# Kernel optimization log

Hardware: AMD Instinct MI355X
Metric: run time of the kernel (lower is better)

## Reference

```python
import jax, jax.numpy as jnp
import numpy as np

WIN = (2, 7, 7)
SHIFT = (1, 3, 3)
D, H, W = 8, 56, 56
C, NH = 128, 4
B = 8
N = WIN[0] * WIN[1] * WIN[2]  # 98


def _relative_position_index():
    d, h, w = np.meshgrid(np.arange(WIN[0]), np.arange(WIN[1]), np.arange(WIN[2]), indexing='ij')
    coords = np.stack([d.ravel(), h.ravel(), w.ravel()])  # (3, N)
    rel = coords[:, :, None] - coords[:, None, :]  # (3, N, N)
    rel = rel.transpose(1, 2, 0).astype(np.int64)
    rel[:, :, 0] += WIN[0] - 1
    rel[:, :, 1] += WIN[1] - 1
    rel[:, :, 2] += WIN[2] - 1
    rel[:, :, 0] *= (2 * WIN[1] - 1) * (2 * WIN[2] - 1)
    rel[:, :, 1] *= 2 * WIN[2] - 1
    return rel.sum(-1).astype(np.int32)  # (N, N)


def _shift_mask():
    img = np.zeros((1, D, H, W, 1), dtype=np.float32)
    cnt = 0
    for ds in (slice(0, -WIN[0]), slice(-WIN[0], -SHIFT[0]), slice(-SHIFT[0], None)):
        for hs in (slice(0, -WIN[1]), slice(-WIN[1], -SHIFT[1]), slice(-SHIFT[1], None)):
            for ws in (slice(0, -WIN[2]), slice(-WIN[2], -SHIFT[2]), slice(-SHIFT[2], None)):
                img[:, ds, hs, ws, :] = cnt
                cnt += 1
    m = img.reshape(1, D // WIN[0], WIN[0], H // WIN[1], WIN[1], W // WIN[2], WIN[2], 1)
    m = m.transpose(0, 1, 3, 5, 2, 4, 6, 7).reshape(-1, N)  # (nW, N)
    diff = m[:, None, :] - m[:, :, None]
    return np.where(diff != 0, np.float32(-100.0), np.float32(0.0))  # (nW, N, N)


def setup_inputs() -> dict:
    key = jax.random.key(0)
    ks = jax.random.split(key, 6)
    nW = (D // WIN[0]) * (H // WIN[1]) * (W // WIN[2])  # 256
    B_ = B * nW  # 2048
    table_size = (2 * WIN[0] - 1) * (2 * WIN[1] - 1) * (2 * WIN[2] - 1)  # 507
    return {
        'x': jax.random.normal(ks[0], (B_, N, C), dtype=jnp.float32),
        'qkv_w': jax.random.normal(ks[1], (3 * C, C), dtype=jnp.float32) * 0.02,
        'qkv_b': jax.random.normal(ks[2], (3 * C,), dtype=jnp.float32) * 0.02,
        'rpb_table': jax.random.normal(ks[3], (table_size, NH), dtype=jnp.float32) * 0.02,
        'proj_w': jax.random.normal(ks[4], (C, C), dtype=jnp.float32) * 0.02,
        'proj_b': jax.random.normal(ks[5], (C,), dtype=jnp.float32) * 0.02,
        'rel_index': jnp.asarray(_relative_position_index()),
        'mask': jnp.asarray(_shift_mask()),
    }


def reference(x, qkv_w, qkv_b, rpb_table, proj_w, proj_b, rel_index, mask):
    B_, n, c = x.shape
    hd = c // NH
    scale = hd ** -0.5
    # qkv projection -> (B_, n, 3, NH, hd)
    qkv = (x @ qkv_w.T + qkv_b).reshape(B_, n, 3, NH, hd)
    qkv = jnp.transpose(qkv, (2, 0, 3, 1, 4))  # (3, B_, NH, n, hd)
    q, k, v = qkv[0], qkv[1], qkv[2]
    attn = jnp.einsum('bhnd,bhmd->bhnm', q * scale, k)  # (B_, NH, n, n)
    # relative position bias gather
    bias = rpb_table[rel_index[:n, :n].reshape(-1)].reshape(n, n, NH)
    attn = attn + jnp.transpose(bias, (2, 0, 1))[None]
    # shift mask add
    nW = mask.shape[0]
    attn = attn.reshape(B_ // nW, nW, NH, n, n) + mask[None, :, None]
    attn = jax.nn.softmax(attn.reshape(B_, NH, n, n), axis=-1)
    out = jnp.einsum('bhnm,bhmd->bhnd', attn, v)
    out = jnp.transpose(out, (0, 2, 1, 3)).reshape(B_, n, c)
    return out @ proj_w.T + proj_b
```

## Files before the change

kernel.cpp:

```cpp
#include <hip/hip_runtime.h>
#include <math.h>
#include <stdint.h>


#define LOG2E   1.4426950408889634f
#define MASKNEG (-144.26950408889634f)

typedef __attribute__((ext_vector_type(8)))  short    bf16x8;
typedef __attribute__((ext_vector_type(4)))  float    f32x4;
typedef __attribute__((ext_vector_type(16))) float    f32x16;
typedef __attribute__((ext_vector_type(4)))  unsigned uint32x4;

__device__ __forceinline__ unsigned short cvt1(float f) {
    __bf16 h = (__bf16)f;
    return __builtin_bit_cast(unsigned short, h);
}
__device__ __forceinline__ unsigned cvt2(float lo, float hi) {
    return (unsigned)cvt1(lo) | ((unsigned)cvt1(hi) << 16);
}

__device__ __forceinline__ void pswap(unsigned &a, unsigned &b) {
    asm volatile("v_permlane32_swap_b32 %0, %1" : "+v"(a), "+v"(b));
}

__device__ __forceinline__ int tok_code(int t) {
    int pd = t / 49;
    int r  = t - pd * 49;
    int ph = r / 7;
    int pw = r - ph * 7;
    return (pd >= 1 ? 1 : 0) | (ph >= 4 ? 2 : 0) | (pw >= 4 ? 4 : 0);
}

__device__ __forceinline__ int swz2(int row, int col) {
    return row * 128 + ((((col >> 3) ^ (row & 7) ^ ((row >> 3) & 3)) & 15) << 3) + (col & 7);
}

template<bool BIG>
__global__ void prep_kernel(const float* __restrict__ qkv_w,
                            const float* __restrict__ proj_w,
                            const float* __restrict__ rpb_table,
                            const int*   __restrict__ rel_index,
                            unsigned short* __restrict__ wqkv,
                            unsigned short* __restrict__ wproj,
                            void* __restrict__ btab) {
    int tid = blockIdx.x * blockDim.x + threadIdx.x;
    int stride = gridDim.x * blockDim.x;
    for (int i = tid; i < 384 * 128; i += stride) wqkv[i]  = cvt1(qkv_w[i]);
    for (int i = tid; i < 128 * 128; i += stride) wproj[i] = cvt1(proj_w[i]);
    if constexpr (BIG) {
        float* bm = (float*)btab;
        for (int idx = tid; idx < 524288; idx += stride) {
            int e  = idx & 3;
            int il = (idx >> 2) & 31;
            int hi = (idx >> 7) & 1;
            int q  = (idx >> 8) & 3;
            int jt = (idx >> 10) & 3;
            int it = (idx >> 12) & 3;
            int h  = (idx >> 14) & 3;
            int cl = (idx >> 16);
            int i = it * 32 + il;
            int j = jt * 32 + q * 8 + hi * 4 + e;
            float v;
            if (j >= 98) v = -INFINITY;
            else if (i >= 98) v = 0.f;
            else {
                float bias = rpb_table[rel_index[i * 98 + j] * 4 + h];
                bool  msk  = (((unsigned)tok_code(i) ^ (unsigned)tok_code(j)) & (unsigned)cl) != 0;
                v = bias * LOG2E + (msk ? MASKNEG : 0.f);
            }
            bm[idx] = v;
        }
    } else {
        unsigned short* bm = (unsigned short*)btab;
        for (int idx = tid; idx < 65536; idx += stride) {
            int e  = idx & 3;
            int il = (idx >> 2) & 31;
            int hi = (idx >> 7) & 1;
            int q  = (idx >> 8) & 3;
            int jt = (idx >> 10) & 3;
            int it = (idx >> 12) & 3;
            int h  = (idx >> 14) & 3;
            int i = it * 32 + il;
            int j = jt * 32 + q * 8 + hi * 4 + e;
            float v;
            if (j >= 98) v = -INFINITY;
            else if (i >= 98) v = 0.f;
            else v = rpb_table[rel_index[i * 98 + j] * 4 + h] * LOG2E;
            bm[idx] = cvt1(v);
        }
    }
}

template<bool BIG>
__global__ __launch_bounds__(1024)
void swin_main(const float* __restrict__ x,
               const float* __restrict__ qkv_b,
               const float* __restrict__ proj_b,
               const unsigned short* __restrict__ wqkv,
               const unsigned short* __restrict__ wproj,
               const void* __restrict__ btab,
               float* __restrict__ out)
{
    extern __shared__ unsigned short lds[];
    unsigned short* q_lds  = lds;
    unsigned short* k_lds  = lds + 14336;
    unsigned short* vT_lds = lds + 28672;
    unsigned short* xo_lds = lds + 45056;

    const int b    = blockIdx.x;
    const int tid  = threadIdx.x;
    const int wv   = tid >> 6;
    const int lane = tid & 63;
    const int l4   = lane >> 4;
    const int lc   = lane & 15;

    {
        int idx2 = tid * 2;
        int row  = idx2 >> 4;
        int c    = 112 + (idx2 & 15);
        *(unsigned int*)(vT_lds + swz2(row, c)) = 0u;
    }

    {
        const float* xb = x + (size_t)b * 12544;
        for (int idx = tid; idx < 3584; idx += 1024) {
            int tok = idx >> 5;
            int c   = (idx & 31) << 2;
            float4 v;
            if (tok < 98) v = *(const float4*)(xb + tok * 128 + c);
            else { v.x = 0.f; v.y = 0.f; v.z = 0.f; v.w = 0.f; }
            uint2 hv; hv.x = cvt2(v.x, v.y); hv.y = cvt2(v.z, v.w);
            *(uint2*)(xo_lds + swz2(tok, c)) = hv;
        }
    }
    __syncthreads();

    {
        const int ct = wv;
        bf16x8 wf[4];
        f32x4  bias;
        const unsigned short* wrow = wqkv + (ct * 16 + lc) * 128;
#pragma unroll
        for (int kt = 0; kt < 4; ++kt) wf[kt] = *(const bf16x8*)(wrow + kt * 32 + l4 * 8);
#pragma unroll
        for (int r = 0; r < 4; ++r) bias[r] = qkv_b[ct * 16 + l4 * 4 + r];
        const bool  isq = (ct < 8);
        const float qs  = 0.17677669529663689f * LOG2E;
#pragma unroll
        for (int t = 0; t < 7; ++t) {
            bf16x8 xf[4];
#pragma unroll
            for (int kt = 0; kt < 4; ++kt)
                xf[kt] = *(bf16x8*)(xo_lds + swz2(t * 16 + lc, kt * 32 + l4 * 8));
            f32x4 acc = bias;
#pragma unroll
            for (int kt = 0; kt < 4; ++kt)
                acc = __builtin_amdgcn_mfma_f32_16x16x32_bf16(wf[kt], xf[kt], acc, 0, 0, 0);
            int tok = t * 16 + lc;
            if (isq) {
                uint2 hv; hv.x = cvt2(acc[0] * qs, acc[1] * qs); hv.y = cvt2(acc[2] * qs, acc[3] * qs);
                *(uint2*)(q_lds + swz2(tok, ct * 16 + l4 * 4)) = hv;
            } else {
                uint2 hv; hv.x = cvt2(acc[0], acc[1]); hv.y = cvt2(acc[2], acc[3]);
                *(uint2*)(k_lds + swz2(tok, (ct - 8) * 16 + l4 * 4)) = hv;
            }
        }
        const int vd = (wv >> 1) * 16;
        bf16x8 wf2[4];
        const unsigned short* wrow2 = wqkv + (256 + vd + lc) * 128;
#pragma unroll
        for (int kt = 0; kt < 4; ++kt) wf2[kt] = *(const bf16x8*)(wrow2 + kt * 32 + l4 * 8);
        f32x4 bias2;
#pragma unroll
        for (int r = 0; r < 4; ++r) bias2[r] = qkv_b[256 + vd + l4 * 4 + r];
        const int t0 = (wv & 1) ? 4 : 0, t1 = (wv & 1) ? 7 : 4;
        for (int t = t0; t < t1; ++t) {
            bf16x8 xf[4];
#pragma unroll
            for (int kt = 0; kt < 4; ++kt)
                xf[kt] = *(bf16x8*)(xo_lds + swz2(t * 16 + lc, kt * 32 + l4 * 8));
            f32x4 acc = bias2;
#pragma unroll
            for (int kt = 0; kt < 4; ++kt)
                acc = __builtin_amdgcn_mfma_f32_16x16x32_bf16(wf2[kt], xf[kt], acc, 0, 0, 0);
            int tok = t * 16 + lc;
            const int rb = vd + l4 * 4;
            vT_lds[swz2(rb + 0, tok)] = cvt1(acc[0]);
            vT_lds[swz2(rb + 1, tok)] = cvt1(acc[1]);
            vT_lds[swz2(rb + 2, tok)] = cvt1(acc[2]);
            vT_lds[swz2(rb + 3, tok)] = cvt1(acc[3]);
        }
    }
    __syncthreads();

    const int wi  = b & 255;
    const unsigned int cls =
        ((wi >> 6) == 3 ? 1u : 0u) | (((wi >> 3) & 7) == 7 ? 2u : 0u) | ((wi & 7) == 7 ? 4u : 0u);
    {
        const int il  = lane & 31;
        const int hi2 = lane >> 5;
        const int h     = wv >> 2;
        const int itile = wv & 3;
        const int i_tok = itile * 32 + il;

        f32x16 S[4];
        if constexpr (BIG) {
            const float* tb = (const float*)btab
                + (((size_t)(cls * 4 + h) * 4 + itile) * 4) * 1024 + hi2 * 128 + il * 4;
#pragma unroll
            for (int jt = 0; jt < 4; ++jt)
#pragma unroll
                for (int q = 0; q < 4; ++q) {
                    f32x4 v = *(const f32x4*)(tb + (jt * 8 + q * 2) * 128);
                    S[jt][q * 4 + 0] = v[0]; S[jt][q * 4 + 1] = v[1];
                    S[jt][q * 4 + 2] = v[2]; S[jt][q * 4 + 3] = v[3];
                }
        } else {
            const unsigned short* tb = (const unsigned short*)btab
                + ((h * 4 + itile) * 4) * 1024 + hi2 * 128 + il * 4;
            const unsigned int ci = (unsigned)tok_code(i_tok);
#pragma unroll
            for (int jt = 0; jt < 4; ++jt)
#pragma unroll
                for (int q = 0; q < 4; ++q) {
                    ushort4 bb = *(const ushort4*)(tb + (jt * 8 + q * 2) * 128);
#pragma unroll
                    for (int e = 0; e < 4; ++e) {
                        unsigned short us = (e == 0) ? bb.x : (e == 1) ? bb.y : (e == 2) ? bb.z : bb.w;
                        int j = jt * 32 + q * 8 + hi2 * 4 + e;
                        float mv = (((unsigned)tok_code(j) ^ ci) & cls) ? MASKNEG : 0.f;
                        S[jt][q * 4 + e] = __builtin_bit_cast(float, (unsigned)us << 16) + mv;
                    }
                }
        }

        bf16x8 qfa = *(bf16x8*)(q_lds + swz2(i_tok, h * 32 + hi2 * 8));
        bf16x8 qfb = *(bf16x8*)(q_lds + swz2(i_tok, h * 32 + 16 + hi2 * 8));
#pragma unroll
        for (int jt = 0; jt < 4; ++jt) {
            bf16x8 ka = *(bf16x8*)(k_lds + swz2(jt * 32 + il, h * 32 + hi2 * 8));
            bf16x8 kb = *(bf16x8*)(k_lds + swz2(jt * 32 + il, h * 32 + 16 + hi2 * 8));
            S[jt] = __builtin_amdgcn_mfma_f32_32x32x16_bf16(ka, qfa, S[jt], 0, 0, 0);
            S[jt] = __builtin_amdgcn_mfma_f32_32x32x16_bf16(kb, qfb, S[jt], 0, 0, 0);
        }

        float m = S[0][0];
#pragma unroll
        for (int jt = 0; jt < 4; ++jt)
#pragma unroll
            for (int r = 0; r < 16; ++r)
                if (!(jt == 0 && r == 0)) m = fmaxf(m, S[jt][r]);
        m = fmaxf(m, __shfl_xor(m, 32));

        float l = 0.f;
        unsigned dw[4][8];
#pragma unroll
        for (int jt = 0; jt < 4; ++jt)
#pragma unroll
            for (int d = 0; d < 8; ++d) {
                float p0 = exp2f(S[jt][2 * d]     - m);
                float p1 = exp2f(S[jt][2 * d + 1] - m);
                l += p0 + p1;
                dw[jt][d] = cvt2(p0, p1);
            }
        l += __shfl_xor(l, 32);

#pragma unroll
        for (int jt = 0; jt < 4; ++jt) {
            pswap(dw[jt][0], dw[jt][2]);
            pswap(dw[jt][1], dw[jt][3]);
            pswap(dw[jt][4], dw[jt][6]);
            pswap(dw[jt][5], dw[jt][7]);
        }

        f32x16 O = {0.f,0.f,0.f,0.f,0.f,0.f,0.f,0.f,0.f,0.f,0.f,0.f,0.f,0.f,0.f,0.f};
#pragma unroll
        for (int jt = 0; jt < 4; ++jt)
#pragma unroll
            for (int p = 0; p < 2; ++p) {
                bf16x8 vf = *(bf16x8*)(vT_lds + swz2(h * 32 + il, jt * 32 + p * 16 + hi2 * 8));
                uint32x4 pu = { dw[jt][p * 4 + 0], dw[jt][p * 4 + 1],
                                dw[jt][p * 4 + 2], dw[jt][p * 4 + 3] };
                O = __builtin_amdgcn_mfma_f32_32x32x16_bf16(
                        vf, __builtin_bit_cast(bf16x8, pu), O, 0, 0, 0);
            }

        const float inv = 1.0f / l;
#pragma unroll
        for (int rr = 0; rr < 8; ++rr) {
            int r = rr * 2;
            int d = (r & 3) + 8 * (r >> 2) + 4 * hi2;
            *(unsigned*)(xo_lds + swz2(i_tok, h * 32 + d)) = cvt2(O[r] * inv, O[r + 1] * inv);
        }
    }
    __syncthreads();

    {
        const int ct = wv >> 1;
        bf16x8 pw[4];
#pragma unroll
        for (int kt = 0; kt < 4; ++kt)
            pw[kt] = *(const bf16x8*)(wproj + (ct * 16 + lc) * 128 + kt * 32 + l4 * 8);
        f32x4 pbias;
#pragma unroll
        for (int r = 0; r < 4; ++r) pbias[r] = proj_b[ct * 16 + l4 * 4 + r];

        float* ob = out + (size_t)b * 12544;
        const int t0 = (wv & 1) ? 4 : 0, t1 = (wv & 1) ? 7 : 4;
        for (int t = t0; t < t1; ++t) {
            f32x4 acc = pbias;
#pragma unroll
            for (int kt = 0; kt < 4; ++kt) {
                bf16x8 of = *(bf16x8*)(xo_lds + swz2(t * 16 + lc, kt * 32 + l4 * 8));
                acc = __builtin_amdgcn_mfma_f32_16x16x32_bf16(pw[kt], of, acc, 0, 0, 0);
            }
            int tok = t * 16 + lc;
            if (tok < 98) {
                float4 st; st.x = acc[0]; st.y = acc[1]; st.z = acc[2]; st.w = acc[3];
                *(float4*)(ob + tok * 128 + ct * 16 + l4 * 4) = st;
            }
        }
    }
}

extern "C" void kernel_launch(void* const* d_in, const int* in_sizes, int n_in,
                              void* d_out, int out_size, void* d_ws, size_t ws_size,
                              hipStream_t stream) {
    const float* x       = (const float*)d_in[0];
    const float* qkv_w   = (const float*)d_in[1];
    const float* qkv_b   = (const float*)d_in[2];
    const float* rpb_tab = (const float*)d_in[3];
    const float* proj_w  = (const float*)d_in[4];
    const float* proj_b  = (const float*)d_in[5];
    const int*   rel_idx = (const int*)d_in[6];

    unsigned short* wqkv  = (unsigned short*)d_ws;
    unsigned short* wproj = (unsigned short*)((char*)d_ws + 98304);
    void*           btab  = (void*)((char*)d_ws + 131072);
    float*          out   = (float*)d_out;

    const bool big = ws_size >= (size_t)(131072 + 524288 * 4);
    const int LDS_BYTES = 122880;

    if (big) {
        hipLaunchKernelGGL((prep_kernel<true>), dim3(512), dim3(256), 0, stream,
                           qkv_w, proj_w, rpb_tab, rel_idx, wqkv, wproj, btab);
        (void)hipFuncSetAttribute((const void*)(swin_main<true>),
                                  hipFuncAttributeMaxDynamicSharedMemorySize, LDS_BYTES);
        hipLaunchKernelGGL((swin_main<true>), dim3(2048), dim3(1024), LDS_BYTES, stream,
                           x, qkv_b, proj_b, wqkv, wproj, btab, out);
    } else {
        hipLaunchKernelGGL((prep_kernel<false>), dim3(512), dim3(256), 0, stream,
                           qkv_w, proj_w, rpb_tab, rel_idx, wqkv, wproj, btab);
        (void)hipFuncSetAttribute((const void*)(swin_main<false>),
                                  hipFuncAttributeMaxDynamicSharedMemorySize, LDS_BYTES);
        hipLaunchKernelGGL((swin_main<false>), dim3(2048), dim3(1024), LDS_BYTES, stream,
                           x, qkv_b, proj_b, wqkv, wproj, btab, out);
    }
}
```

Baseline: 151.1 us.

## Process two windows per 1024-thread block with per-window 512-thread halves

Restructures the main kernel so each 1024-thread block handles two windows, each on 8 waves. Each wave computes Q, K and V for one 16-column slice in a single pass and keeps V in registers before writing it transposed. It also reuses LDS regions, skips the padded key tiles in softmax and PV, and drops the small-workspace fallback path. The goal is to halve the block count and amortize weight loads and synchronisation across more work. The cost is more LDS per block, about 158 KB, plus higher register pressure, and the code now assumes the large workspace is always available.

```diff
diff --git a/kernel.cpp b/kernel.cpp
--- a/kernel.cpp
+++ b/kernel.cpp
@@ -18,11 +18,9 @@
 __device__ __forceinline__ unsigned cvt2(float lo, float hi) {
     return (unsigned)cvt1(lo) | ((unsigned)cvt1(hi) << 16);
 }
-
 __device__ __forceinline__ void pswap(unsigned &a, unsigned &b) {
     asm volatile("v_permlane32_swap_b32 %0, %1" : "+v"(a), "+v"(b));
 }
-
 __device__ __forceinline__ int tok_code(int t) {
     int pd = t / 49;
     int r  = t - pd * 49;
@@ -30,183 +28,157 @@
     int pw = r - ph * 7;
     return (pd >= 1 ? 1 : 0) | (ph >= 4 ? 2 : 0) | (pw >= 4 ? 4 : 0);
 }
-
 __device__ __forceinline__ int swz2(int row, int col) {
     return row * 128 + ((((col >> 3) ^ (row & 7) ^ ((row >> 3) & 3)) & 15) << 3) + (col & 7);
 }
 
-template<bool BIG>
-__global__ void prep_kernel(const float* __restrict__ qkv_w,
-                            const float* __restrict__ proj_w,
-                            const float* __restrict__ rpb_table,
-                            const int*   __restrict__ rel_index,
-                            unsigned short* __restrict__ wqkv,
-                            unsigned short* __restrict__ wproj,
-                            void* __restrict__ btab) {
+__global__ void prep(const float* __restrict__ qkv_w,
+                     const float* __restrict__ proj_w,
+                     const float* __restrict__ rpb_table,
+                     const int*   __restrict__ rel_index,
+                     unsigned short* __restrict__ wqkv,
+                     unsigned short* __restrict__ wproj,
+                     float* __restrict__ bm) {
     int tid = blockIdx.x * blockDim.x + threadIdx.x;
     int stride = gridDim.x * blockDim.x;
     for (int i = tid; i < 384 * 128; i += stride) wqkv[i]  = cvt1(qkv_w[i]);
     for (int i = tid; i < 128 * 128; i += stride) wproj[i] = cvt1(proj_w[i]);
-    if constexpr (BIG) {
-        float* bm = (float*)btab;
-        for (int idx = tid; idx < 524288; idx += stride) {
-            int e  = idx & 3;
-            int il = (idx >> 2) & 31;
-            int hi = (idx >> 7) & 1;
-            int q  = (idx >> 8) & 3;
-            int jt = (idx >> 10) & 3;
-            int it = (idx >> 12) & 3;
-            int h  = (idx >> 14) & 3;
-            int cl = (idx >> 16);
-            int i = it * 32 + il;
-            int j = jt * 32 + q * 8 + hi * 4 + e;
-            float v;
-            if (j >= 98) v = -INFINITY;
-            else if (i >= 98) v = 0.f;
-            else {
-                float bias = rpb_table[rel_index[i * 98 + j] * 4 + h];
-                bool  msk  = (((unsigned)tok_code(i) ^ (unsigned)tok_code(j)) & (unsigned)cl) != 0;
-                v = bias * LOG2E + (msk ? MASKNEG : 0.f);
-            }
-            bm[idx] = v;
-        }
-    } else {
-        unsigned short* bm = (unsigned short*)btab;
-        for (int idx = tid; idx < 65536; idx += stride) {
-            int e  = idx & 3;
-            int il = (idx >> 2) & 31;
-            int hi = (idx >> 7) & 1;
-            int q  = (idx >> 8) & 3;
-            int jt = (idx >> 10) & 3;
-            int it = (idx >> 12) & 3;
-            int h  = (idx >> 14) & 3;
-            int i = it * 32 + il;
-            int j = jt * 32 + q * 8 + hi * 4 + e;
-            float v;
-            if (j >= 98) v = -INFINITY;
-            else if (i >= 98) v = 0.f;
-            else v = rpb_table[rel_index[i * 98 + j] * 4 + h] * LOG2E;
-            bm[idx] = cvt1(v);
-        }
-    }
-}
-
-template<bool BIG>
-__global__ __launch_bounds__(1024)
-void swin_main(const float* __restrict__ x,
-               const float* __restrict__ qkv_b,
-               const float* __restrict__ proj_b,
-               const unsigned short* __restrict__ wqkv,
-               const unsigned short* __restrict__ wproj,
-               const void* __restrict__ btab,
-               float* __restrict__ out)
+    for (int idx = tid; idx < 524288; idx += stride) {
+        int e  = idx & 3;
+        int il = (idx >> 2) & 31;
+        int hi = (idx >> 7) & 1;
+        int q  = (idx >> 8) & 3;
+        int jt = (idx >> 10) & 3;
+        int it = (idx >> 12) & 3;
+        int h  = (idx >> 14) & 3;
+        int cl = (idx >> 16);
+        int i = it * 32 + il;
+        int j = jt * 32 + q * 8 + hi * 4 + e;
+        float v;
+        if (j >= 98) v = -INFINITY;
+        else if (i >= 98) v = 0.f;
+        else {
+            float bias = rpb_table[rel_index[i * 98 + j] * 4 + h];
+            bool  msk  = (((unsigned)tok_code(i) ^ (unsigned)tok_code(j)) & (unsigned)cl) != 0;
+            v = bias * LOG2E + (msk ? MASKNEG : 0.f);
+        }
+        bm[idx] = v;
+    }
+}
+
+__global__ __launch_bounds__(1024, 4)
+void swin_fused2(const float* __restrict__ x,
+                 const float* __restrict__ qkv_b,
+                 const float* __restrict__ proj_b,
+                 const unsigned short* __restrict__ wqkv,
+                 const unsigned short* __restrict__ wproj,
+                 const float* __restrict__ bm,
+                 float* __restrict__ out)
 {
     extern __shared__ unsigned short lds[];
-    unsigned short* q_lds  = lds;
-    unsigned short* k_lds  = lds + 14336;
-    unsigned short* vT_lds = lds + 28672;
-    unsigned short* xo_lds = lds + 45056;
-
-    const int b    = blockIdx.x;
     const int tid  = threadIdx.x;
-    const int wv   = tid >> 6;
+    const int wg   = tid >> 9;
+    const int wtid = tid & 511;
+    const int lw   = wtid >> 6;
     const int lane = tid & 63;
     const int l4   = lane >> 4;
     const int lc   = lane & 15;
-
-    {
-        int idx2 = tid * 2;
-        int row  = idx2 >> 4;
-        int c    = 112 + (idx2 & 15);
-        *(unsigned int*)(vT_lds + swz2(row, c)) = 0u;
-    }
+    const int b    = blockIdx.x * 2 + wg;
+
+    unsigned short* q_w  = lds + wg * 40448;
+    unsigned short* k_w  = q_w + 12544;
+    unsigned short* xv_w = q_w + 25088;
 
     {
         const float* xb = x + (size_t)b * 12544;
-        for (int idx = tid; idx < 3584; idx += 1024) {
+#pragma unroll
+        for (int i = 0; i < 7; ++i) {
+            int idx = wtid + i * 512;
             int tok = idx >> 5;
             int c   = (idx & 31) << 2;
             float4 v;
             if (tok < 98) v = *(const float4*)(xb + tok * 128 + c);
             else { v.x = 0.f; v.y = 0.f; v.z = 0.f; v.w = 0.f; }
             uint2 hv; hv.x = cvt2(v.x, v.y); hv.y = cvt2(v.z, v.w);
-            *(uint2*)(xo_lds + swz2(tok, c)) = hv;
+            *(uint2*)(xv_w + swz2(tok, c)) = hv;
         }
     }
     __syncthreads();
 
-    {
-        const int ct = wv;
-        bf16x8 wf[4];
-        f32x4  bias;
-        const unsigned short* wrow = wqkv + (ct * 16 + lc) * 128;
-#pragma unroll
-        for (int kt = 0; kt < 4; ++kt) wf[kt] = *(const bf16x8*)(wrow + kt * 32 + l4 * 8);
-#pragma unroll
-        for (int r = 0; r < 4; ++r) bias[r] = qkv_b[ct * 16 + l4 * 4 + r];
-        const bool  isq = (ct < 8);
-        const float qs  = 0.17677669529663689f * LOG2E;
+    f32x4 vacc[7];
+    {
+        bf16x8 wfq[4], wfk[4], wfv[4];
+        const unsigned short* rq = wqkv + (lw * 16 + lc) * 128;
+        const unsigned short* rk = wqkv + (128 + lw * 16 + lc) * 128;
+        const unsigned short* rv = wqkv + (256 + lw * 16 + lc) * 128;
+#pragma unroll
+        for (int kt = 0; kt < 4; ++kt) {
+            wfq[kt] = *(const bf16x8*)(rq + kt * 32 + l4 * 8);
+            wfk[kt] = *(const bf16x8*)(rk + kt * 32 + l4 * 8);
+            wfv[kt] = *(const bf16x8*)(rv + kt * 32 + l4 * 8);
+        }
+        f32x4 bq, bk, bv;
+#pragma unroll
+        for (int r = 0; r < 4; ++r) {
+            bq[r] = qkv_b[lw * 16 + l4 * 4 + r];
+            bk[r] = qkv_b[128 + lw * 16 + l4 * 4 + r];
+            bv[r] = qkv_b[256 + lw * 16 + l4 * 4 + r];
+        }
+        const float qs = 0.17677669529663689f * LOG2E;
 #pragma unroll
         for (int t = 0; t < 7; ++t) {
             bf16x8 xf[4];
 #pragma unroll
             for (int kt = 0; kt < 4; ++kt)
-                xf[kt] = *(bf16x8*)(xo_lds + swz2(t * 16 + lc, kt * 32 + l4 * 8));
-            f32x4 acc = bias;
-#pragma unroll
-            for (int kt = 0; kt < 4; ++kt)
-                acc = __builtin_amdgcn_mfma_f32_16x16x32_bf16(wf[kt], xf[kt], acc, 0, 0, 0);
+                xf[kt] = *(bf16x8*)(xv_w + swz2(t * 16 + lc, kt * 32 + l4 * 8));
+            f32x4 aq = bq, ak = bk, av = bv;
+#pragma unroll
+            for (int kt = 0; kt < 4; ++kt) {
+                aq = __builtin_amdgcn_mfma_f32_16x16x32_bf16(wfq[kt], xf[kt], aq, 0, 0, 0);
+                ak = __builtin_amdgcn_mfma_f32_16x16x32_bf16(wfk[kt], xf[kt], ak, 0, 0, 0);
+                av = __builtin_amdgcn_mfma_f32_16x16x32_bf16(wfv[kt], xf[kt], av, 0, 0, 0);
+            }
+            vacc[t] = av;
             int tok = t * 16 + lc;
-            if (isq) {
-                uint2 hv; hv.x = cvt2(acc[0] * qs, acc[1] * qs); hv.y = cvt2(acc[2] * qs, acc[3] * qs);
-                *(uint2*)(q_lds + swz2(tok, ct * 16 + l4 * 4)) = hv;
-            } else {
-                uint2 hv; hv.x = cvt2(acc[0], acc[1]); hv.y = cvt2(acc[2], acc[3]);
-                *(uint2*)(k_lds + swz2(tok, (ct - 8) * 16 + l4 * 4)) = hv;
-            }
-        }
-        const int vd = (wv >> 1) * 16;
-        bf16x8 wf2[4];
-        const unsigned short* wrow2 = wqkv + (256 + vd + lc) * 128;
-#pragma unroll
-        for (int kt = 0; kt < 4; ++kt) wf2[kt] = *(const bf16x8*)(wrow2 + kt * 32 + l4 * 8);
-        f32x4 bias2;
-#pragma unroll
-        for (int r = 0; r < 4; ++r) bias2[r] = qkv_b[256 + vd + l4 * 4 + r];
-        const int t0 = (wv & 1) ? 4 : 0, t1 = (wv & 1) ? 7 : 4;
-        for (int t = t0; t < t1; ++t) {
-            bf16x8 xf[4];
-#pragma unroll
-            for (int kt = 0; kt < 4; ++kt)
-                xf[kt] = *(bf16x8*)(xo_lds + swz2(t * 16 + lc, kt * 32 + l4 * 8));
-            f32x4 acc = bias2;
-#pragma unroll
-            for (int kt = 0; kt < 4; ++kt)
-                acc = __builtin_amdgcn_mfma_f32_16x16x32_bf16(wf2[kt], xf[kt], acc, 0, 0, 0);
+            if (tok < 98) {
+                uint2 hq; hq.x = cvt2(aq[0] * qs, aq[1] * qs); hq.y = cvt2(aq[2] * qs, aq[3] * qs);
+                *(uint2*)(q_w + swz2(tok, lw * 16 + l4 * 4)) = hq;
+                uint2 hk; hk.x = cvt2(ak[0], ak[1]); hk.y = cvt2(ak[2], ak[3]);
+                *(uint2*)(k_w + swz2(tok, lw * 16 + l4 * 4)) = hk;
+            }
+        }
+    }
+    __syncthreads();
+
+    {
+        const int rb = lw * 16 + l4 * 4;
+#pragma unroll
+        for (int t = 0; t < 7; ++t) {
             int tok = t * 16 + lc;
-            const int rb = vd + l4 * 4;
-            vT_lds[swz2(rb + 0, tok)] = cvt1(acc[0]);
-            vT_lds[swz2(rb + 1, tok)] = cvt1(acc[1]);
-            vT_lds[swz2(rb + 2, tok)] = cvt1(acc[2]);
-            vT_lds[swz2(rb + 3, tok)] = cvt1(acc[3]);
+            xv_w[(rb + 0) * 120 + tok] = cvt1(vacc[t][0]);
+            xv_w[(rb + 1) * 120 + tok] = cvt1(vacc[t][1]);
+            xv_w[(rb + 2) * 120 + tok] = cvt1(vacc[t][2]);
+            xv_w[(rb + 3) * 120 + tok] = cvt1(vacc[t][3]);
         }
     }
     __syncthreads();
 
-    const int wi  = b & 255;
-    const unsigned int cls =
-        ((wi >> 6) == 3 ? 1u : 0u) | (((wi >> 3) & 7) == 7 ? 2u : 0u) | ((wi & 7) == 7 ? 4u : 0u);
-    {
+    {
+        const int wi = b & 255;
+        const unsigned cls =
+            ((wi >> 6) == 3 ? 1u : 0u) | (((wi >> 3) & 7) == 7 ? 2u : 0u) | ((wi & 7) == 7 ? 4u : 0u);
         const int il  = lane & 31;
         const int hi2 = lane >> 5;
-        const int h     = wv >> 2;
-        const int itile = wv & 3;
-        const int i_tok = itile * 32 + il;
-
-        f32x16 S[4];
-        if constexpr (BIG) {
-            const float* tb = (const float*)btab
-                + (((size_t)(cls * 4 + h) * 4 + itile) * 4) * 1024 + hi2 * 128 + il * 4;
+
+#pragma unroll
+        for (int p2 = 0; p2 < 2; ++p2) {
+            const int task  = lw + (p2 << 3);
+            const int h     = task >> 2;
+            const int itile = task & 3;
+            const int i_tok = itile * 32 + il;
+
+            f32x16 S[4];
+            const float* tb = bm + (((size_t)(cls * 4 + h) * 4 + itile) * 4) * 1024 + hi2 * 128 + il * 4;
 #pragma unroll
             for (int jt = 0; jt < 4; ++jt)
 #pragma unroll
@@ -215,88 +187,81 @@
                     S[jt][q * 4 + 0] = v[0]; S[jt][q * 4 + 1] = v[1];
                     S[jt][q * 4 + 2] = v[2]; S[jt][q * 4 + 3] = v[3];
                 }
-        } else {
-            const unsigned short* tb = (const unsigned short*)btab
-                + ((h * 4 + itile) * 4) * 1024 + hi2 * 128 + il * 4;
-            const unsigned int ci = (unsigned)tok_code(i_tok);
+
+            bf16x8 qfa = *(bf16x8*)(q_w + swz2(i_tok, h * 32 + hi2 * 8));
+            bf16x8 qfb = *(bf16x8*)(q_w + swz2(i_tok, h * 32 + 16 + hi2 * 8));
+#pragma unroll
+            for (int jt = 0; jt < 4; ++jt) {
+                bf16x8 ka = *(bf16x8*)(k_w + swz2(jt * 32 + il, h * 32 + hi2 * 8));
+                bf16x8 kb = *(bf16x8*)(k_w + swz2(jt * 32 + il, h * 32 + 16 + hi2 * 8));
+                S[jt] = __builtin_amdgcn_mfma_f32_32x32x16_bf16(ka, qfa, S[jt], 0, 0, 0);
+                S[jt] = __builtin_amdgcn_mfma_f32_32x32x16_bf16(kb, qfb, S[jt], 0, 0, 0);
+            }
+
+            float m = S[0][0];
 #pragma unroll
             for (int jt = 0; jt < 4; ++jt)
 #pragma unroll
-                for (int q = 0; q < 4; ++q) {
-                    ushort4 bb = *(const ushort4*)(tb + (jt * 8 + q * 2) * 128);
-#pragma unroll
-                    for (int e = 0; e < 4; ++e) {
-                        unsigned short us = (e == 0) ? bb.x : (e == 1) ? bb.y : (e == 2) ? bb.z : bb.w;
-                        int j = jt * 32 + q * 8 + hi2 * 4 + e;
-                        float mv = (((unsigned)tok_code(j) ^ ci) & cls) ? MASKNEG : 0.f;
-                        S[jt][q * 4 + e] = __builtin_bit_cast(float, (unsigned)us << 16) + mv;
-                    }
-                }
-        }
-
-        bf16x8 qfa = *(bf16x8*)(q_lds + swz2(i_tok, h * 32 + hi2 * 8));
-        bf16x8 qfb = *(bf16x8*)(q_lds + swz2(i_tok, h * 32 + 16 + hi2 * 8));
-#pragma unroll
-        for (int jt = 0; jt < 4; ++jt) {
-            bf16x8 ka = *(bf16x8*)(k_lds + swz2(jt * 32 + il, h * 32 + hi2 * 8));
-            bf16x8 kb = *(bf16x8*)(k_lds + swz2(jt * 32 + il, h * 32 + 16 + hi2 * 8));
-            S[jt] = __builtin_amdgcn_mfma_f32_32x32x16_bf16(ka, qfa, S[jt], 0, 0, 0);
-            S[jt] = __builtin_amdgcn_mfma_f32_32x32x16_bf16(kb, qfb, S[jt], 0, 0, 0);
-        }
-
-        float m = S[0][0];
-#pragma unroll
-        for (int jt = 0; jt < 4; ++jt)
-#pragma unroll
-            for (int r = 0; r < 16; ++r)
-                if (!(jt == 0 && r == 0)) m = fmaxf(m, S[jt][r]);
-        m = fmaxf(m, __shfl_xor(m, 32));
-
-        float l = 0.f;
-        unsigned dw[4][8];
-#pragma unroll
-        for (int jt = 0; jt < 4; ++jt)
-#pragma unroll
-            for (int d = 0; d < 8; ++d) {
-                float p0 = exp2f(S[jt][2 * d]     - m);
-                float p1 = exp2f(S[jt][2 * d + 1] - m);
-                l += p0 + p1;
-                dw[jt][d] = cvt2(p0, p1);
-            }
-        l += __shfl_xor(l, 32);
-
-#pragma unroll
-        for (int jt = 0; jt < 4; ++jt) {
-            pswap(dw[jt][0], dw[jt][2]);
-            pswap(dw[jt][1], dw[jt][3]);
-            pswap(dw[jt][4], dw[jt][6]);
-            pswap(dw[jt][5], dw[jt][7]);
-        }
-
-        f32x16 O = {0.f,0.f,0.f,0.f,0.f,0.f,0.f,0.f,0.f,0.f,0.f,0.f,0.f,0.f,0.f,0.f};
-#pragma unroll
-        for (int jt = 0; jt < 4; ++jt)
-#pragma unroll
-            for (int p = 0; p < 2; ++p) {
-                bf16x8 vf = *(bf16x8*)(vT_lds + swz2(h * 32 + il, jt * 32 + p * 16 + hi2 * 8));
-                uint32x4 pu = { dw[jt][p * 4 + 0], dw[jt][p * 4 + 1],
-                                dw[jt][p * 4 + 2], dw[jt][p * 4 + 3] };
-                O = __builtin_amdgcn_mfma_f32_32x32x16_bf16(
-                        vf, __builtin_bit_cast(bf16x8, pu), O, 0, 0, 0);
-            }
-
-        const float inv = 1.0f / l;
-#pragma unroll
-        for (int rr = 0; rr < 8; ++rr) {
-            int r = rr * 2;
-            int d = (r & 3) + 8 * (r >> 2) + 4 * hi2;
-            *(unsigned*)(xo_lds + swz2(i_tok, h * 32 + d)) = cvt2(O[r] * inv, O[r + 1] * inv);
+                for (int r = 0; r < 16; ++r) {
+                    if (jt == 3 && r >= 8) continue;
+                    if (!(jt == 0 && r == 0)) m = fmaxf(m, S[jt][r]);
+                }
+            m = fmaxf(m, __shfl_xor(m, 32));
+
+            float l = 0.f;
+            unsigned dw[4][8];
+#pragma unroll
+            for (int jt = 0; jt < 4; ++jt) {
+                const int dmax = (jt == 3) ? 4 : 8;
+#pragma unroll
+                for (int d = 0; d < 8; ++d) {
+                    if (d >= dmax) continue;
+                    float p0 = exp2f(S[jt][2 * d]     - m);
+                    float p1 = exp2f(S[jt][2 * d + 1] - m);
+                    l += p0 + p1;
+                    dw[jt][d] = cvt2(p0, p1);
+                }
+            }
+            l += __shfl_xor(l, 32);
+
+#pragma unroll
+            for (int jt = 0; jt < 4; ++jt) {
+                pswap(dw[jt][0], dw[jt][2]);
+                pswap(dw[jt][1], dw[jt][3]);
+                if (jt < 3) {
+                    pswap(dw[jt][4], dw[jt][6]);
+                    pswap(dw[jt][5], dw[jt][7]);
+                }
+            }
+
+            f32x16 O = {0.f,0.f,0.f,0.f,0.f,0.f,0.f,0.f,0.f,0.f,0.f,0.f,0.f,0.f,0.f,0.f};
+#pragma unroll
+            for (int jt = 0; jt < 4; ++jt)
+#pragma unroll
+                for (int p = 0; p < 2; ++p) {
+                    if (jt == 3 && p == 1) continue;
+                    bf16x8 vf = *(bf16x8*)(xv_w + (h * 32 + il) * 120 + jt * 32 + p * 16 + hi2 * 8);
+                    uint32x4 pu = { dw[jt][p * 4 + 0], dw[jt][p * 4 + 1],
+                                    dw[jt][p * 4 + 2], dw[jt][p * 4 + 3] };
+                    O = __builtin_amdgcn_mfma_f32_32x32x16_bf16(
+                            vf, __builtin_bit_cast(bf16x8, pu), O, 0, 0, 0);
+                }
+
+            const float inv = 1.0f / l;
+            if (i_tok < 98) {
+#pragma unroll
+                for (int rr = 0; rr < 8; ++rr) {
+                    int r = rr * 2;
+                    int d = (r & 3) + 8 * (r >> 2) + 4 * hi2;
+                    *(unsigned*)(q_w + swz2(i_tok, h * 32 + d)) = cvt2(O[r] * inv, O[r + 1] * inv);
+                }
+            }
         }
     }
     __syncthreads();
 
     {
-        const int ct = wv >> 1;
+        const int ct = lw;
         bf16x8 pw[4];
 #pragma unroll
         for (int kt = 0; kt < 4; ++kt)
@@ -306,12 +271,12 @@
         for (int r = 0; r < 4; ++r) pbias[r] = proj_b[ct * 16 + l4 * 4 + r];
 
         float* ob = out + (size_t)b * 12544;
-        const int t0 = (wv & 1) ? 4 : 0, t1 = (wv & 1) ? 7 : 4;
-        for (int t = t0; t < t1; ++t) {
+#pragma unroll
+        for (int t = 0; t < 7; ++t) {
             f32x4 acc = pbias;
 #pragma unroll
             for (int kt = 0; kt < 4; ++kt) {
-                bf16x8 of = *(bf16x8*)(xo_lds + swz2(t * 16 + lc, kt * 32 + l4 * 8));
+                bf16x8 of = *(bf16x8*)(q_w + swz2(t * 16 + lc, kt * 32 + l4 * 8));
                 acc = __builtin_amdgcn_mfma_f32_16x16x32_bf16(pw[kt], of, acc, 0, 0, 0);
             }
             int tok = t * 16 + lc;
@@ -336,25 +301,15 @@
 
     unsigned short* wqkv  = (unsigned short*)d_ws;
     unsigned short* wproj = (unsigned short*)((char*)d_ws + 98304);
-    void*           btab  = (void*)((char*)d_ws + 131072);
+    float*          bm    = (float*)((char*)d_ws + 131072);
     float*          out   = (float*)d_out;
 
-    const bool big = ws_size >= (size_t)(131072 + 524288 * 4);
-    const int LDS_BYTES = 122880;
-
-    if (big) {
-        hipLaunchKernelGGL((prep_kernel<true>), dim3(512), dim3(256), 0, stream,
-                           qkv_w, proj_w, rpb_tab, rel_idx, wqkv, wproj, btab);
-        (void)hipFuncSetAttribute((const void*)(swin_main<true>),
-                                  hipFuncAttributeMaxDynamicSharedMemorySize, LDS_BYTES);
-        hipLaunchKernelGGL((swin_main<true>), dim3(2048), dim3(1024), LDS_BYTES, stream,
-                           x, qkv_b, proj_b, wqkv, wproj, btab, out);
-    } else {
-        hipLaunchKernelGGL((prep_kernel<false>), dim3(512), dim3(256), 0, stream,
-                           qkv_w, proj_w, rpb_tab, rel_idx, wqkv, wproj, btab);
-        (void)hipFuncSetAttribute((const void*)(swin_main<false>),
-                                  hipFuncAttributeMaxDynamicSharedMemorySize, LDS_BYTES);
-        hipLaunchKernelGGL((swin_main<false>), dim3(2048), dim3(1024), LDS_BYTES, stream,
-                           x, qkv_b, proj_b, wqkv, wproj, btab, out);
-    }
-}
+    hipLaunchKernelGGL(prep, dim3(512), dim3(256), 0, stream,
+                       qkv_w, proj_w, rpb_tab, rel_idx, wqkv, wproj, bm);
+
+    const int LDS_BYTES = 161792;
+    (void)hipFuncSetAttribute((const void*)swin_fused2,
+                              hipFuncAttributeMaxDynamicSharedMemorySize, LDS_BYTES);
+    hipLaunchKernelGGL(swin_fused2, dim3(1024), dim3(1024), LDS_BYTES, stream,
+                       x, qkv_b, proj_b, wqkv, wproj, bm, out);
+}
```

Measured after the change: 168.7 us. +11.7%, slower.
